# Optimization experiments

Measured on AMD Instinct MI355X. Metric: run time of the kernel, lower is better.

The kernel has to match this reference:

```python
import jax, jax.numpy as jnp
import numpy as np


def setup_inputs() -> dict:
    key = jax.random.key(0)
    k1, k2 = jax.random.split(key)
    B, N, C, Hq, Wq = 4, 10, 256, 32, 32
    Hs, Ws = 32, 32
    return {
        "query_features": jax.random.normal(k1, (B, C, Hq, Wq), dtype=jnp.float32),
        "support_features": jax.random.normal(k2, (N, C, Hs, Ws), dtype=jnp.float32),
        "K": 5,
    }


def reference(query_features, support_features, K):
    B, C, Hq, Wq = query_features.shape
    N, _, Hs, Ws = support_features.shape
    Lq, Ls = Hq * Wq, Hs * Ws

    # [B, Lq, C] -> repeat over N -> [B*N, Lq, C]
    q = query_features.reshape(B, C, Lq).transpose(0, 2, 1)
    q = jnp.broadcast_to(q[:, None], (B, N, Lq, C)).reshape(B * N, Lq, C)
    # [N, C, Ls] -> repeat over B -> [B*N, C, Ls]
    s = support_features.reshape(N, C, Ls)
    s = jnp.broadcast_to(s[None], (B, N, C, Ls)).reshape(B * N, C, Ls)

    # global mean-centering (scalar mean over the whole repeated tensor)
    q = q - q.mean()
    s = s - s.mean()

    # unscaled similarity attention: QK^T -> softmax -> PV
    sim = jnp.einsum("bqc,bcs->bqs", q, s)          # [B*N, Lq, Ls]
    sim = jax.nn.softmax(sim, axis=-1)
    aligned = jnp.einsum("bqs,bcs->bqc", sim, s)    # [B*N, Lq, C]

    # average over K shots per class
    aligned = aligned.reshape(B, N // K, K, Hq, Wq, C).mean(axis=2)
    aligned = aligned.transpose(1, 0, 4, 2, 3)      # [N//K, B, C, Hq, Wq]

    q_out = q.transpose(0, 2, 1).reshape(B, N // K, K, C, Hq, Wq).mean(axis=2)
    # q_out: [B, N//K, C, Hq, Wq]
    return q_out, aligned
```

## Files before the change

kernel.cpp:

```cpp
#include <hip/hip_runtime.h>

#define CQ_ELEMS (4 * 256 * 1024)
#define CS_ELEMS (10 * 256 * 1024)
#define OUT2_OFF 2097152

typedef __attribute__((ext_vector_type(8))) _Float16 f16x8;
typedef __attribute__((ext_vector_type(4))) float f32x4;

#define WS_SH 256
#define SH_ELEMS (10 * 1024 * 256)
#define SV_ELEMS (10 * 256 * 1024)

__device__ __forceinline__ void gload_lds16(const unsigned short* g, unsigned short* l) {
    __builtin_amdgcn_global_load_lds(
        (const __attribute__((address_space(1))) void*)g,
        (__attribute__((address_space(3))) void*)l, 16, 0, 0);
}

__global__ __launch_bounds__(256) void means_kernel(const float* __restrict__ q,
                                                    const float* __restrict__ s,
                                                    float* __restrict__ ws) {
    const int tid = blockIdx.x * 256 + threadIdx.x;
    const int stride = gridDim.x * 256;
    float sq = 0.f, ss = 0.f;
    const float4* q4 = (const float4*)q;
    const float4* s4 = (const float4*)s;
    for (int i = tid; i < CQ_ELEMS / 4; i += stride) {
        float4 v = q4[i];
        sq += (v.x + v.y) + (v.z + v.w);
    }
    for (int i = tid; i < CS_ELEMS / 4; i += stride) {
        float4 v = s4[i];
        ss += (v.x + v.y) + (v.z + v.w);
    }
#pragma unroll
    for (int off = 32; off > 0; off >>= 1) {
        sq += __shfl_down(sq, off, 64);
        ss += __shfl_down(ss, off, 64);
    }
    __shared__ float redq[4], reds[4];
    const int lane = threadIdx.x & 63, wid = threadIdx.x >> 6;
    if (lane == 0) { redq[wid] = sq; reds[wid] = ss; }
    __syncthreads();
    if (threadIdx.x == 0) {
        atomicAdd(&ws[0], (redq[0] + redq[1]) + (redq[2] + redq[3]));
        atomicAdd(&ws[1], (reds[0] + reds[1]) + (reds[2] + reds[3]));
    }
}

__global__ __launch_bounds__(256) void convert_kernel(const float* __restrict__ Q,
                                                      const float* __restrict__ S,
                                                      const float* __restrict__ ws,
                                                      unsigned short* __restrict__ sh,
                                                      unsigned short* __restrict__ sv,
                                                      unsigned short* __restrict__ qt,
                                                      float* __restrict__ out) {
    __shared__ unsigned short Th[32][40];
    const int t = threadIdx.x;
    const int x0 = blockIdx.x << 5;
    const int c0 = blockIdx.y << 5;
    const int z = blockIdx.z;

    const int cl = t >> 3, x4 = (t & 7) << 2;

    if (z < 10) {
        const int n = z;
        const float ms = ws[1] * (1.0f / (float)CS_ELEMS);
        float4 v = *(const float4*)(S + ((size_t)(n * 256 + c0 + cl)) * 1024 + x0 + x4);
        float x[4] = {v.x - ms, v.y - ms, v.z - ms, v.w - ms};
        unsigned short hb[4];
#pragma unroll
        for (int j = 0; j < 4; ++j) {
            _Float16 h = (_Float16)x[j];
            hb[j] = __builtin_bit_cast(unsigned short, h);
            Th[cl][x4 + j] = hb[j];
        }
        *(ushort4*)(sv + ((size_t)(n * 256 + c0 + cl)) * 1024 + x0 + x4) =
            make_ushort4(hb[0], hb[1], hb[2], hb[3]);
        {
            const int lin = (z * 8 + blockIdx.y) * 32 + blockIdx.x;
            const int gid = lin * 256 + t;
            if (gid < 524288) ((int4*)(out + OUT2_OFF))[gid] = make_int4(0, 0, 0, 0);
        }
        __syncthreads();
        const int sl = t >> 3, c4 = (t & 7) << 2;
        *(ushort4*)(sh + ((size_t)(n * 1024 + x0 + sl)) * 256 + c0 + c4) =
            make_ushort4(Th[c4 + 0][sl], Th[c4 + 1][sl], Th[c4 + 2][sl], Th[c4 + 3][sl]);
    } else {
        const int b = z - 10;
        const float mq = ws[0] * (1.0f / (float)CQ_ELEMS);
        float4 v = *(const float4*)(Q + ((size_t)(b * 256 + c0 + cl)) * 1024 + x0 + x4);
        v.x -= mq; v.y -= mq; v.z -= mq; v.w -= mq;
        float* o = out + ((size_t)(b * 2) * 256 + (c0 + cl)) * 1024 + x0 + x4;
        *(float4*)o = v;
        *(float4*)(o + 256 * 1024) = v;
        float x[4] = {v.x, v.y, v.z, v.w};
#pragma unroll
        for (int j = 0; j < 4; ++j) {
            _Float16 h = (_Float16)x[j];
            Th[cl][x4 + j] = __builtin_bit_cast(unsigned short, h);
        }
        __syncthreads();
        const int ql = t >> 3, c4 = (t & 7) << 2;
        *(ushort4*)(qt + ((size_t)(b * 1024 + x0 + ql)) * 256 + c0 + c4) =
            make_ushort4(Th[c4 + 0][ql], Th[c4 + 1][ql], Th[c4 + 2][ql], Th[c4 + 3][ql]);
    }
}

union __align__(16) SMem {
    struct {
        unsigned short s1[8192];
        unsigned short s2[8192];
        unsigned short pb[64][40];
    } st;
    float epi[2][64][68];
};

__global__ __launch_bounds__(256, 3) void attn_kernel(const unsigned short* __restrict__ qt,
                                                      const unsigned short* __restrict__ sh,
                                                      const unsigned short* __restrict__ sv,
                                                      float* __restrict__ out) {
    __shared__ SMem sm;

    const int t = threadIdx.x;
    const int w = t >> 6;
    const int lane = t & 63;
    const int quad = lane >> 4;
    const int l16 = lane & 15;

    int qx, b, n;
    {
        const int L = blockIdx.x;
        if (L < 512) {
            n = L & 7;
            const int inner = L >> 3;
            b = inner & 3;
            qx = inner >> 2;
        } else {
            const int r = L - 512;
            const int x = r & 7;
            n = 8 + (x >> 2);
            const int combo = (x & 3) * 16 + (r >> 3);
            b = combo & 3;
            qx = combo >> 2;
        }
    }
    const int q0 = qx << 6;
    const int g = n / 5;

    const unsigned short* __restrict__ Shn = sh + (size_t)n * (1024 * 256);
    const unsigned short* __restrict__ Svn = sv + (size_t)n * (256 * 1024);

    f16x8 qf[8];
    {
        const unsigned short* qp = qt + (size_t)(b * 1024 + q0 + 16 * w + l16) * 256 + quad * 8;
#pragma unroll
        for (int f = 0; f < 8; ++f)
            qf[f] = *(const f16x8*)(qp + f * 32);
    }

    f16x8 onesA;
#pragma unroll
    for (int j = 0; j < 8; ++j) onesA[j] = (_Float16)1.0f;

    f32x4 O[4][4];
#pragma unroll
    for (int mt = 0; mt < 4; ++mt)
#pragma unroll
        for (int nt = 0; nt < 4; ++nt) O[mt][nt] = (f32x4){0.f, 0.f, 0.f, 0.f};

    f32x4 Lsum[4];
#pragma unroll
    for (int nt = 0; nt < 4; ++nt) Lsum[nt] = (f32x4){0.f, 0.f, 0.f, 0.f};

    float m_run[4];
#pragma unroll
    for (int r = 0; r < 4; ++r) m_run[r] = -1e30f;

    for (int s0i = 0; s0i < 32; ++s0i) {
        const int s0 = s0i << 5;

#pragma unroll
        for (int j = 0; j < 4; ++j) {
            const int fidx = 4 * w + j;
            const unsigned short* g1 = Shn +
                (size_t)(s0 + 2 * (lane & 15) + (fidx & 1)) * 256 + (fidx >> 1) * 32 + (lane >> 4) * 8;
            gload_lds16(g1, &sm.st.s1[fidx * 512]);
            const unsigned short* g2 = Svn +
                (size_t)(w * 64 + j * 16 + (lane >> 2)) * 1024 + s0 + ((lane & 3) ^ (lane >> 4)) * 8;
            gload_lds16(g2, &sm.st.s2[fidx * 512]);
        }
        __syncthreads();

        f32x4 sim0 = (f32x4){0.f, 0.f, 0.f, 0.f};
        f32x4 sim1 = (f32x4){0.f, 0.f, 0.f, 0.f};
#pragma unroll
        for (int f = 0; f < 8; ++f) {
            const unsigned short* base = &sm.st.s1[f * 1024 + quad * 128 + l16 * 8];
            f16x8 b0 = *(const f16x8*)base;
            f16x8 b1 = *(const f16x8*)(base + 512);
            sim0 = __builtin_amdgcn_mfma_f32_16x16x32_f16(qf[f], b0, sim0, 0, 0, 0);
            sim1 = __builtin_amdgcn_mfma_f32_16x16x32_f16(qf[f], b1, sim1, 0, 0, 0);
        }

        float rowmax[4];
#pragma unroll
        for (int r = 0; r < 4; ++r) rowmax[r] = fmaxf(sim0[r], sim1[r]);
#pragma unroll
        for (int off = 1; off <= 8; off <<= 1)
#pragma unroll
            for (int r = 0; r < 4; ++r)
                rowmax[r] = fmaxf(rowmax[r], __shfl_xor(rowmax[r], off, 64));

        float al[4], pv0[4], pv1[4];
#pragma unroll
        for (int r = 0; r < 4; ++r) {
            const float mn = fmaxf(m_run[r], rowmax[r]);
            al[r] = __expf(m_run[r] - mn);
            m_run[r] = mn;
            pv0[r] = __expf(sim0[r] - mn);
            pv1[r] = __expf(sim1[r] - mn);
        }

#pragma unroll
        for (int r = 0; r < 4; ++r) {
            union { _Float16 h[2]; unsigned u; } pk;
            pk.h[0] = (_Float16)pv0[r];
            pk.h[1] = (_Float16)pv1[r];
            *(unsigned*)&sm.st.pb[16 * w + 4 * quad + r][l16 * 2] = pk.u;
        }
        if (l16 == 0) {
#pragma unroll
            for (int r = 0; r < 4; ++r)
                *(float*)&sm.st.pb[16 * w + 4 * quad + r][32] = al[r];
        }
        __syncthreads();

#pragma unroll
        for (int nt = 0; nt < 4; ++nt) {
            const float a = *(const float*)&sm.st.pb[16 * nt + l16][32];
#pragma unroll
            for (int mt = 0; mt < 4; ++mt) {
                O[mt][nt][0] *= a; O[mt][nt][1] *= a; O[mt][nt][2] *= a; O[mt][nt][3] *= a;
            }
            Lsum[nt][0] *= a; Lsum[nt][1] *= a; Lsum[nt][2] *= a; Lsum[nt][3] *= a;
        }
        f16x8 vf[4], pf[4];
#pragma unroll
        for (int mt = 0; mt < 4; ++mt) {
            const int c = 64 * w + 16 * mt + l16;
            const int p = c * 4 + (quad ^ ((l16 >> 2) & 3));
            vf[mt] = *(const f16x8*)&sm.st.s2[p * 8];
        }
#pragma unroll
        for (int nt = 0; nt < 4; ++nt)
            pf[nt] = *(const f16x8*)&sm.st.pb[16 * nt + l16][quad * 8];
#pragma unroll
        for (int mt = 0; mt < 4; ++mt)
#pragma unroll
            for (int nt = 0; nt < 4; ++nt)
                O[mt][nt] = __builtin_amdgcn_mfma_f32_16x16x32_f16(vf[mt], pf[nt], O[mt][nt], 0, 0, 0);
#pragma unroll
        for (int nt = 0; nt < 4; ++nt)
            Lsum[nt] = __builtin_amdgcn_mfma_f32_16x16x32_f16(onesA, pf[nt], Lsum[nt], 0, 0, 0);
    }

    __syncthreads();

    float linv[4];
#pragma unroll
    for (int nt = 0; nt < 4; ++nt)
        linv[nt] = 0.2f / Lsum[nt][0];

    float* __restrict__ out2 = out + OUT2_OFF + (size_t)((g << 2) + b) * (256 * 1024);

#pragma unroll
    for (int h = 0; h < 2; ++h) {
        if ((w >> 1) == h) {
            const int we = w & 1;
#pragma unroll
            for (int mt = 0; mt < 4; ++mt)
#pragma unroll
                for (int nt = 0; nt < 4; ++nt)
#pragma unroll
                    for (int r = 0; r < 4; ++r)
                        sm.epi[we][16 * mt + 4 * quad + r][16 * nt + l16] = O[mt][nt][r] * linv[nt];
        }
        __syncthreads();
#pragma unroll 4
        for (int i = 0; i < 32; ++i) {
            const int ro = w * 32 + i;
            const float v = sm.epi[ro >> 6][ro & 63][lane];
            atomicAdd(out2 + (size_t)(h * 128 + ro) * 1024 + q0 + lane, v);
        }
        __syncthreads();
    }
}

extern "C" void kernel_launch(void* const* d_in, const int* in_sizes, int n_in,
                              void* d_out, int out_size, void* d_ws, size_t ws_size,
                              hipStream_t stream) {
    const float* q = (const float*)d_in[0];
    const float* s = (const float*)d_in[1];
    float* out = (float*)d_out;
    float* ws = (float*)d_ws;
    unsigned short* sh = (unsigned short*)((char*)d_ws + WS_SH);
    unsigned short* sv = sh + SH_ELEMS;
    unsigned short* qt = sv + SV_ELEMS;

    hipMemsetAsync(d_ws, 0, 2 * sizeof(float), stream);

    means_kernel<<<256, 256, 0, stream>>>(q, s, ws);
    convert_kernel<<<dim3(32, 8, 14), 256, 0, stream>>>(q, s, ws, sh, sv, qt, out);
    attn_kernel<<<640, 256, 0, stream>>>(qt, sh, sv, out);
}
```

Baseline: 189.7 us.

## Split attention output channels across two blocks to double grid and occupancy

Each attention block now computes only half of the 256 output channels, chosen by a new index h, so the grid grows from 640 to 1280 blocks. The V tile in LDS and the O accumulators are halved, and launch bounds rise to 4 blocks per SM to raise occupancy. The epilogue becomes a single pass without the two-phase staging. In exchange, each pair of blocks recomputes the same QK^T and softmax and reloads the same support tile, doubling that part of the work.

```diff
diff --git a/kernel.cpp b/kernel.cpp
--- a/kernel.cpp
+++ b/kernel.cpp
@@ -110,13 +110,13 @@
 union __align__(16) SMem {
     struct {
         unsigned short s1[8192];
-        unsigned short s2[8192];
+        unsigned short s2[4096];
         unsigned short pb[64][40];
     } st;
-    float epi[2][64][68];
+    float epi[128][66];
 };
 
-__global__ __launch_bounds__(256, 3) void attn_kernel(const unsigned short* __restrict__ qt,
+__global__ __launch_bounds__(256, 4) void attn_kernel(const unsigned short* __restrict__ qt,
                                                       const unsigned short* __restrict__ sh,
                                                       const unsigned short* __restrict__ sv,
                                                       float* __restrict__ out) {
@@ -128,21 +128,23 @@
     const int quad = lane >> 4;
     const int l16 = lane & 15;
 
-    int qx, b, n;
+    int qx, b, n, h;
     {
         const int L = blockIdx.x;
-        if (L < 512) {
+        if (L < 1024) {
             n = L & 7;
             const int inner = L >> 3;
-            b = inner & 3;
-            qx = inner >> 2;
+            h = inner & 1;
+            b = (inner >> 1) & 3;
+            qx = inner >> 3;
         } else {
-            const int r = L - 512;
+            const int r = L - 1024;
             const int x = r & 7;
             n = 8 + (x >> 2);
-            const int combo = (x & 3) * 16 + (r >> 3);
-            b = combo & 3;
-            qx = combo >> 2;
+            const int combo = (x & 3) * 32 + (r >> 3);
+            h = combo & 1;
+            b = (combo >> 1) & 3;
+            qx = combo >> 3;
         }
     }
     const int q0 = qx << 6;
@@ -163,9 +165,9 @@
 #pragma unroll
     for (int j = 0; j < 8; ++j) onesA[j] = (_Float16)1.0f;
 
-    f32x4 O[4][4];
-#pragma unroll
-    for (int mt = 0; mt < 4; ++mt)
+    f32x4 O[2][4];
+#pragma unroll
+    for (int mt = 0; mt < 2; ++mt)
 #pragma unroll
         for (int nt = 0; nt < 4; ++nt) O[mt][nt] = (f32x4){0.f, 0.f, 0.f, 0.f};
 
@@ -186,8 +188,12 @@
             const unsigned short* g1 = Shn +
                 (size_t)(s0 + 2 * (lane & 15) + (fidx & 1)) * 256 + (fidx >> 1) * 32 + (lane >> 4) * 8;
             gload_lds16(g1, &sm.st.s1[fidx * 512]);
+        }
+#pragma unroll
+        for (int j = 0; j < 2; ++j) {
+            const int fidx = 2 * w + j;
             const unsigned short* g2 = Svn +
-                (size_t)(w * 64 + j * 16 + (lane >> 2)) * 1024 + s0 + ((lane & 3) ^ (lane >> 4)) * 8;
+                (size_t)(128 * h + w * 32 + j * 16 + (lane >> 2)) * 1024 + s0 + ((lane & 3) ^ (lane >> 4)) * 8;
             gload_lds16(g2, &sm.st.s2[fidx * 512]);
         }
         __syncthreads();
@@ -224,9 +230,9 @@
 
 #pragma unroll
         for (int r = 0; r < 4; ++r) {
-            union { _Float16 h[2]; unsigned u; } pk;
-            pk.h[0] = (_Float16)pv0[r];
-            pk.h[1] = (_Float16)pv1[r];
+            union { _Float16 hh[2]; unsigned u; } pk;
+            pk.hh[0] = (_Float16)pv0[r];
+            pk.hh[1] = (_Float16)pv1[r];
             *(unsigned*)&sm.st.pb[16 * w + 4 * quad + r][l16 * 2] = pk.u;
         }
         if (l16 == 0) {
@@ -240,15 +246,15 @@
         for (int nt = 0; nt < 4; ++nt) {
             const float a = *(const float*)&sm.st.pb[16 * nt + l16][32];
 #pragma unroll
-            for (int mt = 0; mt < 4; ++mt) {
+            for (int mt = 0; mt < 2; ++mt) {
                 O[mt][nt][0] *= a; O[mt][nt][1] *= a; O[mt][nt][2] *= a; O[mt][nt][3] *= a;
             }
             Lsum[nt][0] *= a; Lsum[nt][1] *= a; Lsum[nt][2] *= a; Lsum[nt][3] *= a;
         }
-        f16x8 vf[4], pf[4];
-#pragma unroll
-        for (int mt = 0; mt < 4; ++mt) {
-            const int c = 64 * w + 16 * mt + l16;
+        f16x8 vf[2], pf[4];
+#pragma unroll
+        for (int mt = 0; mt < 2; ++mt) {
+            const int c = 32 * w + 16 * mt + l16;
             const int p = c * 4 + (quad ^ ((l16 >> 2) & 3));
             vf[mt] = *(const f16x8*)&sm.st.s2[p * 8];
         }
@@ -256,7 +262,7 @@
         for (int nt = 0; nt < 4; ++nt)
             pf[nt] = *(const f16x8*)&sm.st.pb[16 * nt + l16][quad * 8];
 #pragma unroll
-        for (int mt = 0; mt < 4; ++mt)
+        for (int mt = 0; mt < 2; ++mt)
 #pragma unroll
             for (int nt = 0; nt < 4; ++nt)
                 O[mt][nt] = __builtin_amdgcn_mfma_f32_16x16x32_f16(vf[mt], pf[nt], O[mt][nt], 0, 0, 0);
@@ -275,25 +281,17 @@
     float* __restrict__ out2 = out + OUT2_OFF + (size_t)((g << 2) + b) * (256 * 1024);
 
 #pragma unroll
-    for (int h = 0; h < 2; ++h) {
-        if ((w >> 1) == h) {
-            const int we = w & 1;
-#pragma unroll
-            for (int mt = 0; mt < 4; ++mt)
-#pragma unroll
-                for (int nt = 0; nt < 4; ++nt)
-#pragma unroll
-                    for (int r = 0; r < 4; ++r)
-                        sm.epi[we][16 * mt + 4 * quad + r][16 * nt + l16] = O[mt][nt][r] * linv[nt];
-        }
-        __syncthreads();
+    for (int mt = 0; mt < 2; ++mt)
+#pragma unroll
+        for (int nt = 0; nt < 4; ++nt)
+#pragma unroll
+            for (int r = 0; r < 4; ++r)
+                sm.epi[32 * w + 16 * mt + 4 * quad + r][16 * nt + l16] = O[mt][nt][r] * linv[nt];
+    __syncthreads();
 #pragma unroll 4
-        for (int i = 0; i < 32; ++i) {
-            const int ro = w * 32 + i;
-            const float v = sm.epi[ro >> 6][ro & 63][lane];
-            atomicAdd(out2 + (size_t)(h * 128 + ro) * 1024 + q0 + lane, v);
-        }
-        __syncthreads();
+    for (int i = 0; i < 32; ++i) {
+        const int ro = w * 32 + i;
+        atomicAdd(out2 + (size_t)(128 * h + ro) * 1024 + q0 + lane, sm.epi[ro][lane]);
     }
 }
 
@@ -312,5 +310,5 @@
 
     means_kernel<<<256, 256, 0, stream>>>(q, s, ws);
     convert_kernel<<<dim3(32, 8, 14), 256, 0, stream>>>(q, s, ws, sh, sv, qt, out);
-    attn_kernel<<<640, 256, 0, stream>>>(qt, sh, sv, out);
-}
+    attn_kernel<<<1280, 256, 0, stream>>>(qt, sh, sv, out);
+}
```

Result: slower. 257.9 us (+36.0%).

## Double the key tile to 64 per iteration in flash attention loop

Applied to the files above, without the earlier changes.

Each main-loop iteration now processes 64 support positions instead of 32, which halves the iteration count and with it the number of block barriers, softmax rescale passes and shuffle reductions. The LDS staging buffers double in size, the V tile swizzle changes to an 8-way XOR, and the P buffer widens. Occupancy hint drops from 3 to 2 blocks per CU because of the higher LDS and register use, which may reduce latency hiding.

```diff
diff --git a/kernel.cpp b/kernel.cpp
--- a/kernel.cpp
+++ b/kernel.cpp
@@ -109,14 +109,14 @@
 
 union __align__(16) SMem {
     struct {
-        unsigned short s1[8192];
-        unsigned short s2[8192];
-        unsigned short pb[64][40];
+        unsigned short s1[16384];
+        unsigned short s2[16384];
+        unsigned short pb[64][72];
     } st;
     float epi[2][64][68];
 };
 
-__global__ __launch_bounds__(256, 3) void attn_kernel(const unsigned short* __restrict__ qt,
+__global__ __launch_bounds__(256, 2) void attn_kernel(const unsigned short* __restrict__ qt,
                                                       const unsigned short* __restrict__ sh,
                                                       const unsigned short* __restrict__ sv,
                                                       float* __restrict__ out) {
@@ -177,92 +177,117 @@
 #pragma unroll
     for (int r = 0; r < 4; ++r) m_run[r] = -1e30f;
 
-    for (int s0i = 0; s0i < 32; ++s0i) {
-        const int s0 = s0i << 5;
-
-#pragma unroll
-        for (int j = 0; j < 4; ++j) {
-            const int fidx = 4 * w + j;
+    for (int s0i = 0; s0i < 16; ++s0i) {
+        const int s0 = s0i << 6;
+
+#pragma unroll
+        for (int j = 0; j < 8; ++j) {
+            const int fidx = 8 * w + j;
+            const int half = fidx >> 4, f = (fidx >> 1) & 7, ntp = fidx & 1;
             const unsigned short* g1 = Shn +
-                (size_t)(s0 + 2 * (lane & 15) + (fidx & 1)) * 256 + (fidx >> 1) * 32 + (lane >> 4) * 8;
+                (size_t)(s0 + 32 * half + 2 * l16 + ntp) * 256 + f * 32 + quad * 8;
             gload_lds16(g1, &sm.st.s1[fidx * 512]);
-            const unsigned short* g2 = Svn +
-                (size_t)(w * 64 + j * 16 + (lane >> 2)) * 1024 + s0 + ((lane & 3) ^ (lane >> 4)) * 8;
+        }
+#pragma unroll
+        for (int j = 0; j < 8; ++j) {
+            const int fidx = 8 * w + j;
+            const int c = 64 * w + 8 * j + (lane >> 3);
+            const int chunk = (lane & 7) ^ ((lane >> 3) & 7);
+            const unsigned short* g2 = Svn + (size_t)c * 1024 + s0 + chunk * 8;
             gload_lds16(g2, &sm.st.s2[fidx * 512]);
         }
         __syncthreads();
 
-        f32x4 sim0 = (f32x4){0.f, 0.f, 0.f, 0.f};
-        f32x4 sim1 = (f32x4){0.f, 0.f, 0.f, 0.f};
+        f32x4 sA0 = (f32x4){0.f, 0.f, 0.f, 0.f};
+        f32x4 sA1 = (f32x4){0.f, 0.f, 0.f, 0.f};
+        f32x4 sB0 = (f32x4){0.f, 0.f, 0.f, 0.f};
+        f32x4 sB1 = (f32x4){0.f, 0.f, 0.f, 0.f};
 #pragma unroll
         for (int f = 0; f < 8; ++f) {
-            const unsigned short* base = &sm.st.s1[f * 1024 + quad * 128 + l16 * 8];
-            f16x8 b0 = *(const f16x8*)base;
-            f16x8 b1 = *(const f16x8*)(base + 512);
-            sim0 = __builtin_amdgcn_mfma_f32_16x16x32_f16(qf[f], b0, sim0, 0, 0, 0);
-            sim1 = __builtin_amdgcn_mfma_f32_16x16x32_f16(qf[f], b1, sim1, 0, 0, 0);
+            const unsigned short* baseA = &sm.st.s1[f * 1024 + quad * 128 + l16 * 8];
+            const unsigned short* baseB = baseA + 8192;
+            sA0 = __builtin_amdgcn_mfma_f32_16x16x32_f16(qf[f], *(const f16x8*)baseA, sA0, 0, 0, 0);
+            sA1 = __builtin_amdgcn_mfma_f32_16x16x32_f16(qf[f], *(const f16x8*)(baseA + 512), sA1, 0, 0, 0);
+            sB0 = __builtin_amdgcn_mfma_f32_16x16x32_f16(qf[f], *(const f16x8*)baseB, sB0, 0, 0, 0);
+            sB1 = __builtin_amdgcn_mfma_f32_16x16x32_f16(qf[f], *(const f16x8*)(baseB + 512), sB1, 0, 0, 0);
         }
 
         float rowmax[4];
 #pragma unroll
-        for (int r = 0; r < 4; ++r) rowmax[r] = fmaxf(sim0[r], sim1[r]);
+        for (int r = 0; r < 4; ++r)
+            rowmax[r] = fmaxf(fmaxf(sA0[r], sA1[r]), fmaxf(sB0[r], sB1[r]));
 #pragma unroll
         for (int off = 1; off <= 8; off <<= 1)
 #pragma unroll
             for (int r = 0; r < 4; ++r)
                 rowmax[r] = fmaxf(rowmax[r], __shfl_xor(rowmax[r], off, 64));
 
-        float al[4], pv0[4], pv1[4];
+        float al[4], pA0[4], pA1[4], pB0[4], pB1[4];
 #pragma unroll
         for (int r = 0; r < 4; ++r) {
             const float mn = fmaxf(m_run[r], rowmax[r]);
             al[r] = __expf(m_run[r] - mn);
             m_run[r] = mn;
-            pv0[r] = __expf(sim0[r] - mn);
-            pv1[r] = __expf(sim1[r] - mn);
+            pA0[r] = __expf(sA0[r] - mn);
+            pA1[r] = __expf(sA1[r] - mn);
+            pB0[r] = __expf(sB0[r] - mn);
+            pB1[r] = __expf(sB1[r] - mn);
         }
 
 #pragma unroll
         for (int r = 0; r < 4; ++r) {
-            union { _Float16 h[2]; unsigned u; } pk;
-            pk.h[0] = (_Float16)pv0[r];
-            pk.h[1] = (_Float16)pv1[r];
-            *(unsigned*)&sm.st.pb[16 * w + 4 * quad + r][l16 * 2] = pk.u;
+            union { _Float16 h[2]; unsigned u; } pkA, pkB;
+            pkA.h[0] = (_Float16)pA0[r];
+            pkA.h[1] = (_Float16)pA1[r];
+            pkB.h[0] = (_Float16)pB0[r];
+            pkB.h[1] = (_Float16)pB1[r];
+            *(unsigned*)&sm.st.pb[16 * w + 4 * quad + r][l16 * 2] = pkA.u;
+            *(unsigned*)&sm.st.pb[16 * w + 4 * quad + r][32 + l16 * 2] = pkB.u;
         }
         if (l16 == 0) {
 #pragma unroll
             for (int r = 0; r < 4; ++r)
-                *(float*)&sm.st.pb[16 * w + 4 * quad + r][32] = al[r];
+                *(float*)&sm.st.pb[16 * w + 4 * quad + r][64] = al[r];
         }
         __syncthreads();
 
 #pragma unroll
         for (int nt = 0; nt < 4; ++nt) {
-            const float a = *(const float*)&sm.st.pb[16 * nt + l16][32];
+            const float a = *(const float*)&sm.st.pb[16 * nt + l16][64];
 #pragma unroll
             for (int mt = 0; mt < 4; ++mt) {
                 O[mt][nt][0] *= a; O[mt][nt][1] *= a; O[mt][nt][2] *= a; O[mt][nt][3] *= a;
             }
             Lsum[nt][0] *= a; Lsum[nt][1] *= a; Lsum[nt][2] *= a; Lsum[nt][3] *= a;
         }
-        f16x8 vf[4], pf[4];
+
+        f16x8 vf[4][2], pf[4][2];
 #pragma unroll
         for (int mt = 0; mt < 4; ++mt) {
             const int c = 64 * w + 16 * mt + l16;
-            const int p = c * 4 + (quad ^ ((l16 >> 2) & 3));
-            vf[mt] = *(const f16x8*)&sm.st.s2[p * 8];
+#pragma unroll
+            for (int ks = 0; ks < 2; ++ks) {
+                const int p = c * 8 + ((ks * 4 + quad) ^ (c & 7));
+                vf[mt][ks] = *(const f16x8*)&sm.st.s2[p * 8];
+            }
         }
 #pragma unroll
         for (int nt = 0; nt < 4; ++nt)
-            pf[nt] = *(const f16x8*)&sm.st.pb[16 * nt + l16][quad * 8];
+#pragma unroll
+            for (int ks = 0; ks < 2; ++ks)
+                pf[nt][ks] = *(const f16x8*)&sm.st.pb[16 * nt + l16][ks * 32 + quad * 8];
 #pragma unroll
         for (int mt = 0; mt < 4; ++mt)
 #pragma unroll
-            for (int nt = 0; nt < 4; ++nt)
-                O[mt][nt] = __builtin_amdgcn_mfma_f32_16x16x32_f16(vf[mt], pf[nt], O[mt][nt], 0, 0, 0);
-#pragma unroll
-        for (int nt = 0; nt < 4; ++nt)
-            Lsum[nt] = __builtin_amdgcn_mfma_f32_16x16x32_f16(onesA, pf[nt], Lsum[nt], 0, 0, 0);
+            for (int nt = 0; nt < 4; ++nt) {
+                O[mt][nt] = __builtin_amdgcn_mfma_f32_16x16x32_f16(vf[mt][0], pf[nt][0], O[mt][nt], 0, 0, 0);
+                O[mt][nt] = __builtin_amdgcn_mfma_f32_16x16x32_f16(vf[mt][1], pf[nt][1], O[mt][nt], 0, 0, 0);
+            }
+#pragma unroll
+        for (int nt = 0; nt < 4; ++nt) {
+            Lsum[nt] = __builtin_amdgcn_mfma_f32_16x16x32_f16(onesA, pf[nt][0], Lsum[nt], 0, 0, 0);
+            Lsum[nt] = __builtin_amdgcn_mfma_f32_16x16x32_f16(onesA, pf[nt][1], Lsum[nt], 0, 0, 0);
+        }
     }
 
     __syncthreads();
```

Result: slower. 219.2 us (+15.6%).
